# Kernel tuning notes

Hardware: AMD Instinct MI355X
Metric: run time of the kernel (lower is better)

Reference implementation:

```python
import jax, jax.numpy as jnp
import numpy as np


def setup_inputs() -> dict:
    key = jax.random.key(0)
    kx, kw = jax.random.split(key)
    x = jax.random.normal(kx, (32, 256, 56, 56), dtype=jnp.float32)
    weight = jax.random.uniform(kw, (256, 256, 3, 3), dtype=jnp.float32) * 0.001
    return {"x": x, "weight": weight}


def reference(x, weight):
    # --- binarize activations with straight-through estimator ---
    # forward value = sign(x); gradient flows through clamp(x, -1, 1)
    clipped_x = jnp.clip(x, -1.0, 1.0)
    bx = jax.lax.stop_gradient(jnp.sign(x) - clipped_x) + clipped_x

    # --- binarize weights (per-output-channel mean-centered, scaled sign) ---
    w = weight
    # subtract per-output-channel mean over (in_c, kh, kw)
    bw = w - jnp.mean(w.reshape(w.shape[0], -1), axis=-1)[:, None, None, None]
    # per-output-channel scaling factor = mean |bw| (detached)
    scale = jnp.mean(jnp.abs(bw), axis=(1, 2, 3), keepdims=True)
    scale = jax.lax.stop_gradient(scale)
    clipped_w = jnp.clip(bw, -1.0, 1.0)
    binary_w = jax.lax.stop_gradient(scale * jnp.sign(bw) - clipped_w) + clipped_w

    # --- conv2d, NCHW / OIHW, stride 1, padding 1 ---
    y = jax.lax.conv_general_dilated(
        bx, binary_w,
        window_strides=(1, 1),
        padding=((1, 1), (1, 1)),
        dimension_numbers=("NCHW", "OIHW", "NCHW"),
    )
    return y
```

## Files before the change

### kernel.cpp

```cpp
#include <hip/hip_runtime.h>
#include <cstdint>
#include <cstddef>

#define N_ 32
#define C_ 256
#define H_ 56
#define W_ 56

typedef int v4i __attribute__((ext_vector_type(4)));

static constexpr size_t SX_BYTES = (size_t)N_ * 58 * 68 * 256;
static constexpr size_t WB_OFF   = SX_BYTES;
static constexpr size_t WB_BYTES = 36ull * 16 * 64 * 16;
static constexpr size_t SC_OFF   = WB_OFF + WB_BYTES;

__global__ __launch_bounds__(256) void zero_halo(char* __restrict__ sx) {
    int row = blockIdx.x;
    int n   = blockIdx.y;
    v4i z = {0, 0, 0, 0};
    char* base = sx + ((size_t)n * 58 + row) * (68 * 256);
    if (row == 0 || row == 57) {
        for (int i = threadIdx.x; i < 58 * 16; i += 256)
            *(v4i*)(base + (size_t)i * 16) = z;
    } else {
        int tid = threadIdx.x;
        if (tid < 32) {
            int wpos = (tid >> 4) * 57;
            int ch   = tid & 15;
            *(v4i*)(base + ((size_t)wpos * 16 + ch) * 16) = z;
        }
    }
}

__global__ __launch_bounds__(256) void pack_x(const float* __restrict__ x,
                                              char* __restrict__ sx) {
    __shared__ float tile[64 * 65];
    __shared__ char  ob[64 * 256];
    int tid = threadIdx.x;
    int hw0 = blockIdx.x * 64;
    int n   = blockIdx.y;

    int cl   = tid >> 6, hwl = tid & 63;
    int hwl2 = tid >> 2, cq  = tid & 3;

    for (int cb = 0; cb < 4; ++cb) {
        const float* xb = x + ((size_t)n * C_ + cb * 64) * 3136 + hw0;
#pragma unroll
        for (int i = 0; i < 16; ++i) {
            int cloc = i * 4 + cl;
            tile[cloc * 65 + hwl] = xb[(size_t)cloc * 3136 + hwl];
        }
        __syncthreads();
        int words[4];
#pragma unroll
        for (int g = 0; g < 4; ++g) {
            int word = 0;
#pragma unroll
            for (int b = 0; b < 4; ++b) {
                float v = tile[(cq * 16 + g * 4 + b) * 65 + hwl2];
                int s = (v > 0.0f) - (v < 0.0f);
                word |= (s & 0xff) << (8 * b);
            }
            words[g] = word;
        }
        v4i o4 = {words[0], words[1], words[2], words[3]};
        int ch   = cb * 4 + cq;
        int slot = (ch + hwl2) & 15;
        *(v4i*)(ob + hwl2 * 256 + slot * 16) = o4;
        __syncthreads();
    }

#pragma unroll
    for (int j = 0; j < 4; ++j) {
        int i = tid + j * 256;
        int hwl3 = i >> 4, ch = i & 15;
        v4i v = *(const v4i*)(ob + hwl3 * 256 + ((ch + hwl3) & 15) * 16);
        int hw = hw0 + hwl3;
        int h = hw / 56, w = hw - h * 56;
        int slot = (ch + (w + 1)) & 15;
        *(v4i*)(sx + (((size_t)n * 58 + h + 1) * 68 + (w + 1)) * 256 + slot * 16) = v;
    }
}

__global__ __launch_bounds__(256) void pack_w(const float* __restrict__ wt,
                                              char* __restrict__ wB,
                                              float* __restrict__ scaleg) {
    __shared__ double red[256];
    int o = blockIdx.x, tid = threadIdx.x;
    const float* wo = wt + (size_t)o * 2304;

    double s = 0;
    for (int j = tid; j < 2304; j += 256) s += (double)wo[j];
    red[tid] = s;
    __syncthreads();
    for (int k = 128; k > 0; k >>= 1) {
        if (tid < k) red[tid] += red[tid + k];
        __syncthreads();
    }
    double mean = red[0] / 2304.0;
    __syncthreads();

    double s2 = 0;
    for (int j = tid; j < 2304; j += 256) s2 += fabs((double)wo[j] - mean);
    red[tid] = s2;
    __syncthreads();
    for (int k = 128; k > 0; k >>= 1) {
        if (tid < k) red[tid] += red[tid + k];
        __syncthreads();
    }
    if (tid == 0) scaleg[o] = (float)(red[0] / 2304.0);

    if (tid < 144) {
        int kiter = tid >> 2, q = tid & 3;
        int tap = kiter >> 2, cb = kiter & 3;
        int kh = tap / 3, kw = tap - kh * 3;
        int words[4];
        for (int g = 0; g < 4; ++g) {
            int word = 0;
            for (int b = 0; b < 4; ++b) {
                int c = cb * 64 + q * 16 + g * 4 + b;
                double v = (double)wo[c * 9 + kh * 3 + kw];
                int sg = (v > mean) - (v < mean);
                word |= (sg & 0xff) << (8 * b);
            }
            words[g] = word;
        }
        v4i pk = {words[0], words[1], words[2], words[3]};
        *(v4i*)(wB + (((size_t)kiter * 16 + (o >> 4)) * 64 + q * 16 + (o & 15)) * 16) = pk;
    }
}

__global__ __launch_bounds__(256, 2) void conv_mfma(const char* __restrict__ sx,
                                                    const v4i* __restrict__ wB,
                                                    const float* __restrict__ scaleg,
                                                    float* __restrict__ out) {
    __shared__ char xs[4 * 58 * 256];
    int tid = threadIdx.x;
    int wave = tid >> 6, lane = tid & 63;
    int hp = blockIdx.x, n = blockIdx.y;
    int h0 = hp * 2;

    const char* src = sx + ((size_t)n * 58 + h0) * (68 * 256);
    for (int i = tid; i < 4 * 58 * 16; i += 256) {
        int pos = i >> 4;
        int row = pos / 58;
        int w   = pos - row * 58;
        v4i v = *(const v4i*)(src + ((size_t)(row * 68 + w) << 8) + ((size_t)(i & 15) << 4));
        *(v4i*)(xs + (size_t)i * 16) = v;
    }

    int lm = lane & 15, q = lane >> 4;

    int wof[7], ro[7];
#pragma unroll
    for (int mf = 0; mf < 7; ++mf) {
        int m = mf * 16 + lm;
        int r = (m >= 56) ? 1 : 0;
        ro[mf]  = r;
        wof[mf] = m - 56 * r;
    }

    v4i acc[7][4];
#pragma unroll
    for (int mf = 0; mf < 7; ++mf)
#pragma unroll
        for (int of = 0; of < 4; ++of) { v4i z = {0, 0, 0, 0}; acc[mf][of] = z; }

    const v4i* wBw = wB + (size_t)(wave * 4) * 64 + lane;

    __syncthreads();

    v4i bA[4], bB[4], aA[7], aB[7];

#pragma unroll
    for (int of = 0; of < 4; ++of) bA[of] = wBw[of * 64];
    {
        int cbq = q;
#pragma unroll
        for (int mf = 0; mf < 7; ++mf) {
            int win  = wof[mf];
            int pos  = ro[mf] * 58 + win;
            int phys = (pos << 4) | ((cbq + win) & 15);
            aA[mf] = *(const v4i*)(xs + ((size_t)phys << 4));
        }
    }

    for (int k2 = 0; k2 < 18; ++k2) {
        int k0 = 2 * k2, k1 = k0 + 1;
#pragma unroll
        for (int of = 0; of < 4; ++of) bB[of] = wBw[(size_t)k1 * 1024 + of * 64];
        {
            int tap = k1 >> 2, cb = k1 & 3;
            int dh = tap / 3, dw = tap - dh * 3;
            int cbq = cb * 4 + q;
#pragma unroll
            for (int mf = 0; mf < 7; ++mf) {
                int win  = wof[mf] + dw;
                int pos  = (dh + ro[mf]) * 58 + win;
                int phys = (pos << 4) | ((cbq + win) & 15);
                aB[mf] = *(const v4i*)(xs + ((size_t)phys << 4));
            }
        }
#pragma unroll
        for (int mf = 0; mf < 7; ++mf)
#pragma unroll
            for (int of = 0; of < 4; ++of)
                acc[mf][of] = __builtin_amdgcn_mfma_i32_16x16x64_i8(
                    aA[mf], bA[of], acc[mf][of], 0, 0, 0);
        if (k2 < 17) {
            int kn = k0 + 2;
#pragma unroll
            for (int of = 0; of < 4; ++of) bA[of] = wBw[(size_t)kn * 1024 + of * 64];
            int tap = kn >> 2, cb = kn & 3;
            int dh = tap / 3, dw = tap - dh * 3;
            int cbq = cb * 4 + q;
#pragma unroll
            for (int mf = 0; mf < 7; ++mf) {
                int win  = wof[mf] + dw;
                int pos  = (dh + ro[mf]) * 58 + win;
                int phys = (pos << 4) | ((cbq + win) & 15);
                aA[mf] = *(const v4i*)(xs + ((size_t)phys << 4));
            }
        }
#pragma unroll
        for (int mf = 0; mf < 7; ++mf)
#pragma unroll
            for (int of = 0; of < 4; ++of)
                acc[mf][of] = __builtin_amdgcn_mfma_i32_16x16x64_i8(
                    aB[mf], bB[of], acc[mf][of], 0, 0, 0);
    }

#pragma unroll
    for (int of = 0; of < 4; ++of) {
        int o = (wave * 4 + of) * 16 + lm;
        float s = scaleg[o];
#pragma unroll
        for (int mf = 0; mf < 7; ++mf) {
            int m  = mf * 16 + q * 4;
            int r  = (m >= 56) ? 1 : 0;
            int wb = m - 56 * r;
            float* ob = out + ((size_t)(n * C_ + o) * H_ + h0 + r) * W_ + wb;
            float4 v = {s * (float)acc[mf][of].x, s * (float)acc[mf][of].y,
                        s * (float)acc[mf][of].z, s * (float)acc[mf][of].w};
            *(float4*)ob = v;
        }
    }
}

extern "C" void kernel_launch(void* const* d_in, const int* in_sizes, int n_in,
                              void* d_out, int out_size, void* d_ws, size_t ws_size,
                              hipStream_t stream) {
    const float* x   = (const float*)d_in[0];
    const float* wgt = (const float*)d_in[1];
    float* out = (float*)d_out;
    char* ws = (char*)d_ws;

    char*  sx = ws;
    char*  wb = ws + WB_OFF;
    float* sg = (float*)(ws + SC_OFF);

    zero_halo<<<dim3(58, N_), dim3(256), 0, stream>>>(sx);
    pack_x<<<dim3(49, N_), dim3(256), 0, stream>>>(x, sx);
    pack_w<<<dim3(256), dim3(256), 0, stream>>>(wgt, wb, sg);
    conv_mfma<<<dim3(28, N_), dim3(256), 0, stream>>>(sx, (const v4i*)wb, sg, out);
}
```

Before: 248.2 us.

## Split conv block into 8 waves across pixel groups with MFMA priority hints

Doubles the conv block to 512 threads, so each wave handles 4 output-channel fragments over half the pixel rows (4 or 3 M-fragments) instead of all 7. This cuts per-wave accumulator registers, which should allow higher occupancy. The explicit A-fragment double buffering is dropped and MFMA bursts are wrapped in s_setprio. The trade-off is that each wave now re-reads its weight fragments from global memory on its own, doubling weight traffic per block, and there is less software prefetch of LDS operands.

```diff
diff --git a/kernel.cpp b/kernel.cpp
--- a/kernel.cpp
+++ b/kernel.cpp
@@ -130,7 +130,101 @@
     }
 }
 
-__global__ __launch_bounds__(256, 2) void conv_mfma(const char* __restrict__ sx,
+template<int NMF>
+__device__ __forceinline__ void conv_work(const char* xs, const v4i* wBw,
+                                          int mbase, int lm, int q,
+                                          int og, int n, int h0,
+                                          const float* __restrict__ scaleg,
+                                          float* __restrict__ out) {
+    int wof[NMF], ro[NMF];
+#pragma unroll
+    for (int mf = 0; mf < NMF; ++mf) {
+        int m = mbase + mf * 16 + lm;
+        int r = (m >= 56) ? 1 : 0;
+        ro[mf]  = r;
+        wof[mf] = m - 56 * r;
+    }
+
+    v4i acc[NMF][4];
+#pragma unroll
+    for (int mf = 0; mf < NMF; ++mf)
+#pragma unroll
+        for (int of = 0; of < 4; ++of) { v4i z = {0, 0, 0, 0}; acc[mf][of] = z; }
+
+    v4i bA[4], bB[4];
+#pragma unroll
+    for (int of = 0; of < 4; ++of) bA[of] = wBw[of * 64];
+
+    for (int k2 = 0; k2 < 18; ++k2) {
+        int k0 = 2 * k2, k1 = k0 + 1;
+#pragma unroll
+        for (int of = 0; of < 4; ++of) bB[of] = wBw[(size_t)k1 * 1024 + of * 64];
+        {
+            int tap = k0 >> 2, cb = k0 & 3;
+            int dh = tap / 3, dw = tap - dh * 3;
+            int cbq = cb * 4 + q;
+            v4i a[NMF];
+#pragma unroll
+            for (int mf = 0; mf < NMF; ++mf) {
+                int win  = wof[mf] + dw;
+                int pos  = (dh + ro[mf]) * 58 + win;
+                int phys = (pos << 4) | ((cbq + win) & 15);
+                a[mf] = *(const v4i*)(xs + ((size_t)phys << 4));
+            }
+            __builtin_amdgcn_s_setprio(1);
+#pragma unroll
+            for (int mf = 0; mf < NMF; ++mf)
+#pragma unroll
+                for (int of = 0; of < 4; ++of)
+                    acc[mf][of] = __builtin_amdgcn_mfma_i32_16x16x64_i8(
+                        a[mf], bA[of], acc[mf][of], 0, 0, 0);
+            __builtin_amdgcn_s_setprio(0);
+        }
+        if (k2 < 17) {
+#pragma unroll
+            for (int of = 0; of < 4; ++of) bA[of] = wBw[(size_t)(k0 + 2) * 1024 + of * 64];
+        }
+        {
+            int tap = k1 >> 2, cb = k1 & 3;
+            int dh = tap / 3, dw = tap - dh * 3;
+            int cbq = cb * 4 + q;
+            v4i a[NMF];
+#pragma unroll
+            for (int mf = 0; mf < NMF; ++mf) {
+                int win  = wof[mf] + dw;
+                int pos  = (dh + ro[mf]) * 58 + win;
+                int phys = (pos << 4) | ((cbq + win) & 15);
+                a[mf] = *(const v4i*)(xs + ((size_t)phys << 4));
+            }
+            __builtin_amdgcn_s_setprio(1);
+#pragma unroll
+            for (int mf = 0; mf < NMF; ++mf)
+#pragma unroll
+                for (int of = 0; of < 4; ++of)
+                    acc[mf][of] = __builtin_amdgcn_mfma_i32_16x16x64_i8(
+                        a[mf], bB[of], acc[mf][of], 0, 0, 0);
+            __builtin_amdgcn_s_setprio(0);
+        }
+    }
+
+#pragma unroll
+    for (int of = 0; of < 4; ++of) {
+        int o = og * 64 + of * 16 + lm;
+        float s = scaleg[o];
+#pragma unroll
+        for (int mf = 0; mf < NMF; ++mf) {
+            int m  = mbase + mf * 16 + q * 4;
+            int r  = (m >= 56) ? 1 : 0;
+            int wb = m - 56 * r;
+            float* ob = out + ((size_t)(n * C_ + o) * H_ + h0 + r) * W_ + wb;
+            float4 v = {s * (float)acc[mf][of].x, s * (float)acc[mf][of].y,
+                        s * (float)acc[mf][of].z, s * (float)acc[mf][of].w};
+            *(float4*)ob = v;
+        }
+    }
+}
+
+__global__ __launch_bounds__(512, 4) void conv_mfma(const char* __restrict__ sx,
                                                     const v4i* __restrict__ wB,
                                                     const float* __restrict__ scaleg,
                                                     float* __restrict__ out) {
@@ -141,7 +235,7 @@
     int h0 = hp * 2;
 
     const char* src = sx + ((size_t)n * 58 + h0) * (68 * 256);
-    for (int i = tid; i < 4 * 58 * 16; i += 256) {
+    for (int i = tid; i < 4 * 58 * 16; i += 512) {
         int pos = i >> 4;
         int row = pos / 58;
         int w   = pos - row * 58;
@@ -150,101 +244,18 @@
     }
 
     int lm = lane & 15, q = lane >> 4;
-
-    int wof[7], ro[7];
-#pragma unroll
-    for (int mf = 0; mf < 7; ++mf) {
-        int m = mf * 16 + lm;
-        int r = (m >= 56) ? 1 : 0;
-        ro[mf]  = r;
-        wof[mf] = m - 56 * r;
-    }
-
-    v4i acc[7][4];
-#pragma unroll
-    for (int mf = 0; mf < 7; ++mf)
-#pragma unroll
-        for (int of = 0; of < 4; ++of) { v4i z = {0, 0, 0, 0}; acc[mf][of] = z; }
-
-    const v4i* wBw = wB + (size_t)(wave * 4) * 64 + lane;
-
-    __syncthreads();
-
-    v4i bA[4], bB[4], aA[7], aB[7];
-
-#pragma unroll
-    for (int of = 0; of < 4; ++of) bA[of] = wBw[of * 64];
-    {
-        int cbq = q;
-#pragma unroll
-        for (int mf = 0; mf < 7; ++mf) {
-            int win  = wof[mf];
-            int pos  = ro[mf] * 58 + win;
-            int phys = (pos << 4) | ((cbq + win) & 15);
-            aA[mf] = *(const v4i*)(xs + ((size_t)phys << 4));
-        }
-    }
-
-    for (int k2 = 0; k2 < 18; ++k2) {
-        int k0 = 2 * k2, k1 = k0 + 1;
-#pragma unroll
-        for (int of = 0; of < 4; ++of) bB[of] = wBw[(size_t)k1 * 1024 + of * 64];
-        {
-            int tap = k1 >> 2, cb = k1 & 3;
-            int dh = tap / 3, dw = tap - dh * 3;
-            int cbq = cb * 4 + q;
-#pragma unroll
-            for (int mf = 0; mf < 7; ++mf) {
-                int win  = wof[mf] + dw;
-                int pos  = (dh + ro[mf]) * 58 + win;
-                int phys = (pos << 4) | ((cbq + win) & 15);
-                aB[mf] = *(const v4i*)(xs + ((size_t)phys << 4));
-            }
-        }
-#pragma unroll
-        for (int mf = 0; mf < 7; ++mf)
-#pragma unroll
-            for (int of = 0; of < 4; ++of)
-                acc[mf][of] = __builtin_amdgcn_mfma_i32_16x16x64_i8(
-                    aA[mf], bA[of], acc[mf][of], 0, 0, 0);
-        if (k2 < 17) {
-            int kn = k0 + 2;
-#pragma unroll
-            for (int of = 0; of < 4; ++of) bA[of] = wBw[(size_t)kn * 1024 + of * 64];
-            int tap = kn >> 2, cb = kn & 3;
-            int dh = tap / 3, dw = tap - dh * 3;
-            int cbq = cb * 4 + q;
-#pragma unroll
-            for (int mf = 0; mf < 7; ++mf) {
-                int win  = wof[mf] + dw;
-                int pos  = (dh + ro[mf]) * 58 + win;
-                int phys = (pos << 4) | ((cbq + win) & 15);
-                aA[mf] = *(const v4i*)(xs + ((size_t)phys << 4));
-            }
-        }
-#pragma unroll
-        for (int mf = 0; mf < 7; ++mf)
-#pragma unroll
-            for (int of = 0; of < 4; ++of)
-                acc[mf][of] = __builtin_amdgcn_mfma_i32_16x16x64_i8(
-                    aB[mf], bB[of], acc[mf][of], 0, 0, 0);
-    }
-
-#pragma unroll
-    for (int of = 0; of < 4; ++of) {
-        int o = (wave * 4 + of) * 16 + lm;
-        float s = scaleg[o];
-#pragma unroll
-        for (int mf = 0; mf < 7; ++mf) {
-            int m  = mf * 16 + q * 4;
-            int r  = (m >= 56) ? 1 : 0;
-            int wb = m - 56 * r;
-            float* ob = out + ((size_t)(n * C_ + o) * H_ + h0 + r) * W_ + wb;
-            float4 v = {s * (float)acc[mf][of].x, s * (float)acc[mf][of].y,
-                        s * (float)acc[mf][of].z, s * (float)acc[mf][of].w};
-            *(float4*)ob = v;
-        }
-    }
+    int og = wave & 3;
+    int mg = wave >> 2;
+
+    const v4i* wBw = wB + (size_t)(og * 4) * 64 + lane;
+
+    __syncthreads();
+
+    if (mg == 0)
+        conv_work<4>(xs, wBw, 0,  lane & 15, lane >> 4, og, n, h0, scaleg, out);
+    else
+        conv_work<3>(xs, wBw, 64, lane & 15, lane >> 4, og, n, h0, scaleg, out);
+    (void)lm; (void)q;
 }
 
 extern "C" void kernel_launch(void* const* d_in, const int* in_sizes, int n_in,
@@ -262,5 +273,5 @@
     zero_halo<<<dim3(58, N_), dim3(256), 0, stream>>>(sx);
     pack_x<<<dim3(49, N_), dim3(256), 0, stream>>>(x, sx);
     pack_w<<<dim3(256), dim3(256), 0, stream>>>(wgt, wb, sg);
-    conv_mfma<<<dim3(28, N_), dim3(256), 0, stream>>>(sx, (const v4i*)wb, sg, out);
-}
+    conv_mfma<<<dim3(28, N_), dim3(512), 0, stream>>>(sx, (const v4i*)wb, sg, out);
+}
```

After: 262.7 us. 5.9% more time.
